# Performance work log

Hardware: AMD Instinct MI355X
Metric: run time of the kernel (lower is better)

## Reference

```python
import jax, jax.numpy as jnp
import numpy as np

N = 50000      # nodes
E = 800000     # edges
P = 100000     # pos/neg candidate edges
IN = 128       # input feat dim
H, D = 2, 64   # heads, out_feats per head
HD = H * D     # 128
NEG_SLOPE = 0.2


def setup_inputs() -> dict:
    key = jax.random.key(0)
    ks = jax.random.split(key, 18)
    def gn(k, shape, fan_in):
        return jax.random.normal(k, shape, jnp.float32) * (1.0 / np.sqrt(fan_in))
    return {
        "x": jax.random.normal(ks[0], (N, IN), jnp.float32),
        "src": jax.random.randint(ks[1], (E,), 0, N),
        "dst": jax.random.randint(ks[2], (E,), 0, N),
        "pos_src": jax.random.randint(ks[3], (P,), 0, N),
        "pos_dst": jax.random.randint(ks[4], (P,), 0, N),
        "neg_src": jax.random.randint(ks[5], (P,), 0, N),
        "neg_dst": jax.random.randint(ks[6], (P,), 0, N),
        "W0": gn(ks[7], (IN, HD), IN),
        "attn0": gn(ks[8], (H, D), D),
        "W1": gn(ks[9], (HD, HD), HD),
        "attn1": gn(ks[10], (H, D), D),
        "Wp1": gn(ks[11], (HD, D), HD),
        "bp1": jnp.zeros((D,), jnp.float32),
        "Wp2": gn(ks[12], (D, D), D),
        "bp2": jnp.zeros((D,), jnp.float32),
        "Wp3": gn(ks[13], (D, 1), D),
        "bp3": jnp.zeros((1,), jnp.float32),
    }


def gatv2_layer(h, W, attn, src, dst, residual):
    # DGL GATv2Conv, share_weights=True, bias=False, feat_drop=attn_drop=0
    feat = (h @ W).reshape(N, H, D)            # [N,H,D]
    el = feat[src]                              # [E,H,D] gather at src
    er = feat[dst]                              # [E,H,D] gather at dst
    e = jax.nn.leaky_relu(el + er, NEG_SLOPE)   # [E,H,D]
    score = jnp.einsum('ehd,hd->eh', e, attn)   # [E,H]
    # edge softmax over incoming edges of each dst node
    m = jax.ops.segment_max(score, dst, num_segments=N)      # [N,H]
    p = jnp.exp(score - m[dst])                               # [E,H]
    s = jax.ops.segment_sum(p, dst, num_segments=N)           # [N,H]
    a = p / s[dst]                                             # [E,H]
    rst = jax.ops.segment_sum(el * a[:, :, None], dst, num_segments=N)  # [N,H,D]
    if residual:
        rst = rst + h.reshape(N, H, D)          # identity res_fc (dims match)
    return jax.nn.elu(rst).reshape(N, HD)       # flatten(1)


def reference(x, src, dst, pos_src, pos_dst, neg_src, neg_dst,
              W0, attn0, W1, attn1, Wp1, bp1, Wp2, bp2, Wp3, bp3):
    h = gatv2_layer(x, W0, attn0, src, dst, residual=False)
    h = gatv2_layer(h, W1, attn1, src, dst, residual=True)

    def predictor(z):
        z = jax.nn.relu(z @ Wp1 + bp1)
        z = jax.nn.relu(z @ Wp2 + bp2)
        return z @ Wp3 + bp3

    h_pos = predictor(h[pos_src] * h[pos_dst])  # [P,1]
    h_neg = predictor(h[neg_src] * h[neg_dst])  # [P,1]
    return (h_pos, h_neg)
```

## Files before the change

### kernel.cpp

```cpp
#include <hip/hip_runtime.h>
#include <math.h>

#define NN 50000
#define NE 800000
#define NP 100000
#define NEG_SLOPE 0.2f

__device__ __forceinline__ float row_sum16(float v) {
    int x = __float_as_int(v);
    v += __int_as_float(__builtin_amdgcn_update_dpp(0, x, 0x128, 0xF, 0xF, true));
    x = __float_as_int(v);
    v += __int_as_float(__builtin_amdgcn_update_dpp(0, x, 0x124, 0xF, 0xF, true));
    x = __float_as_int(v);
    v += __int_as_float(__builtin_amdgcn_update_dpp(0, x, 0x4E, 0xF, 0xF, true));
    x = __float_as_int(v);
    v += __int_as_float(__builtin_amdgcn_update_dpp(0, x, 0xB1, 0xF, 0xF, true));
    return v;
}


__global__ void count_deg(const int* __restrict__ dst, int* __restrict__ cnt) {
    int i = blockIdx.x * blockDim.x + threadIdx.x;
    int st = gridDim.x * blockDim.x;
    for (; i < NE; i += st) atomicAdd(&cnt[dst[i]], 1);
}

__global__ __launch_bounds__(1024) void scan_deg(const int* __restrict__ cnt,
                                                 int* __restrict__ rowptr,
                                                 int* __restrict__ cursor) {
    __shared__ int wsum[16];
    __shared__ int carry;
    __shared__ int total;
    int tid = threadIdx.x;
    int lane = tid & 63, w = tid >> 6;
    if (tid == 0) carry = 0;
    __syncthreads();
    for (int base = 0; base < NN; base += 1024) {
        int idx = base + tid;
        int v = (idx < NN) ? cnt[idx] : 0;
        int x = v;
        #pragma unroll
        for (int mm = 1; mm < 64; mm <<= 1) {
            int y = __shfl_up(x, mm, 64);
            if (lane >= mm) x += y;
        }
        if (lane == 63) wsum[w] = x;
        __syncthreads();
        if (w == 0) {
            int orig = (lane < 16) ? wsum[lane] : 0;
            int t = orig;
            #pragma unroll
            for (int mm = 1; mm < 16; mm <<= 1) {
                int y = __shfl_up(t, mm, 64);
                if (lane >= mm) t += y;
            }
            if (lane < 16) wsum[lane] = t - orig;
            if (lane == 15) total = t;
        }
        __syncthreads();
        int excl = carry + wsum[w] + x - v;
        if (idx < NN) { rowptr[idx] = excl; cursor[idx] = excl; }
        __syncthreads();
        if (tid == 0) carry += total;
        __syncthreads();
    }
    if (tid == 0) rowptr[NN] = carry;
}

__global__ void scatter_edges(const int* __restrict__ src, const int* __restrict__ dst,
                              int* __restrict__ cursor, int* __restrict__ csrc) {
    int i = blockIdx.x * blockDim.x + threadIdx.x;
    int st = gridDim.x * blockDim.x;
    for (; i < NE; i += st) {
        int p = atomicAdd(&cursor[dst[i]], 1);
        csrc[p] = src[i];
    }
}


__global__ __launch_bounds__(256) void gemm128(const float* __restrict__ A,
                                               const float* __restrict__ W,
                                               float* __restrict__ out, int nrows) {
    __shared__ float Wt[128 * 132];
    __shared__ float rb[16 * 132];
    int tid = threadIdx.x;
    for (int idx = tid; idx < 128 * 128; idx += 256) {
        int k = idx >> 7, j = idx & 127;
        Wt[j * 132 + k] = W[idx];
    }
    __syncthreads();
    int lane = tid & 63, w = tid >> 6;
    int ntiles = (nrows + 15) >> 4;
    const float* w0p = &Wt[lane * 132];
    const float* w1p = &Wt[(64 + lane) * 132];
    for (int t = blockIdx.x; t < ntiles; t += gridDim.x) {
        int r0 = t << 4;
        for (int i = tid; i < 512; i += 256) {
            int rr = r0 + (i >> 5);
            float4 v = {0.f, 0.f, 0.f, 0.f};
            if (rr < nrows) v = ((const float4*)A)[(size_t)rr * 32 + (i & 31)];
            *(float4*)&rb[(i >> 5) * 132 + (i & 31) * 4] = v;
        }
        __syncthreads();
        float acc[4][2] = {};
        #pragma unroll 4
        for (int k4 = 0; k4 < 32; ++k4) {
            float4 wv0 = *(const float4*)&w0p[k4 * 4];
            float4 wv1 = *(const float4*)&w1p[k4 * 4];
            #pragma unroll
            for (int i2 = 0; i2 < 4; ++i2) {
                float4 av = *(const float4*)&rb[(w * 4 + i2) * 132 + k4 * 4];
                acc[i2][0] = fmaf(av.x, wv0.x, acc[i2][0]);
                acc[i2][0] = fmaf(av.y, wv0.y, acc[i2][0]);
                acc[i2][0] = fmaf(av.z, wv0.z, acc[i2][0]);
                acc[i2][0] = fmaf(av.w, wv0.w, acc[i2][0]);
                acc[i2][1] = fmaf(av.x, wv1.x, acc[i2][1]);
                acc[i2][1] = fmaf(av.y, wv1.y, acc[i2][1]);
                acc[i2][1] = fmaf(av.z, wv1.z, acc[i2][1]);
                acc[i2][1] = fmaf(av.w, wv1.w, acc[i2][1]);
            }
        }
        #pragma unroll
        for (int i2 = 0; i2 < 4; ++i2) {
            int rr = r0 + w * 4 + i2;
            if (rr < nrows) {
                out[(size_t)rr * 128 + lane]      = acc[i2][0];
                out[(size_t)rr * 128 + 64 + lane] = acc[i2][1];
            }
        }
        __syncthreads();
    }
}


__global__ void gat_fused(const float* __restrict__ feat,
                          const int* __restrict__ rowptr,
                          const int* __restrict__ csrc,
                          const float* __restrict__ attn,
                          const float* __restrict__ resid,
                          float* __restrict__ out) {
    int tid = blockIdx.x * blockDim.x + threadIdx.x;
    int hw = tid >> 5;
    int nhw = (gridDim.x * blockDim.x) >> 5;
    int q = threadIdx.x & 31;
    const float4* feat4 = (const float4*)feat;
    float4 at = ((const float4*)attn)[q];
    for (int d = hw; d < NN; d += nhw) {
        int beg = rowptr[d], end = rowptr[d + 1];
        float4 fd = feat4[(size_t)d * 32 + q];
        float m = 0.f, s = 0.f;
        float ax = 0.f, ay = 0.f, az = 0.f, aw = 0.f;
        bool first = true;
        int i = beg;
        float4 f0 = {0.f,0.f,0.f,0.f}, f1 = {0.f,0.f,0.f,0.f}, f2 = {0.f,0.f,0.f,0.f};
        if (i     < end) f0 = feat4[(size_t)csrc[i]     * 32 + q];
        if (i + 1 < end) f1 = feat4[(size_t)csrc[i + 1] * 32 + q];
        if (i + 2 < end) f2 = feat4[(size_t)csrc[i + 2] * 32 + q];
        int s3 = (i + 3 < end) ? csrc[i + 3] : 0;
        while (i < end) {
            float4 f3 = {0.f, 0.f, 0.f, 0.f};
            if (i + 3 < end) f3 = feat4[(size_t)s3 * 32 + q];
            int s4 = (i + 4 < end) ? csrc[i + 4] : 0;
            float ex = f0.x + fd.x; ex = ex > 0.f ? ex : NEG_SLOPE * ex;
            float ey = f0.y + fd.y; ey = ey > 0.f ? ey : NEG_SLOPE * ey;
            float ez = f0.z + fd.z; ez = ez > 0.f ? ez : NEG_SLOPE * ez;
            float ew = f0.w + fd.w; ew = ew > 0.f ? ew : NEG_SLOPE * ew;
            float part = ex * at.x + ey * at.y + ez * at.z + ew * at.w;
            part = row_sum16(part);
            float p = first ? 1.f : __expf(part - m);
            m = first ? part : m;
            first = false;
            s += p;
            ax = fmaf(f0.x, p, ax);
            ay = fmaf(f0.y, p, ay);
            az = fmaf(f0.z, p, az);
            aw = fmaf(f0.w, p, aw);
            f0 = f1; f1 = f2; f2 = f3; s3 = s4; ++i;
        }
        float inv = s > 0.f ? 1.f / s : 0.f;
        float vx = ax * inv;
        float vy = ay * inv;
        float vz = az * inv;
        float vw = aw * inv;
        if (resid) {
            float4 r = ((const float4*)resid)[(size_t)d * 32 + q];
            vx += r.x; vy += r.y; vz += r.z; vw += r.w;
        }
        vx = vx > 0.f ? vx : expm1f(vx);
        vy = vy > 0.f ? vy : expm1f(vy);
        vz = vz > 0.f ? vz : expm1f(vz);
        vw = vw > 0.f ? vw : expm1f(vw);
        float4 o; o.x = vx; o.y = vy; o.z = vz; o.w = vw;
        ((float4*)out)[(size_t)d * 32 + q] = o;
    }
}


__global__ __launch_bounds__(512, 1) void predictor(const float* __restrict__ h,
                          const int* __restrict__ ps, const int* __restrict__ pd,
                          const int* __restrict__ ns, const int* __restrict__ nd,
                          const float* __restrict__ Wp1, const float* __restrict__ bp1,
                          const float* __restrict__ Wp2, const float* __restrict__ bp2,
                          const float* __restrict__ Wp3, const float* __restrict__ bp3,
                          float* __restrict__ out) {
    __shared__ float S[29696];
    int tid = threadIdx.x;
    for (int idx = tid; idx < 128 * 64; idx += 512) {
        int k = idx >> 6, c = idx & 63;
        S[c * 132 + k] = Wp1[idx];
    }
    for (int idx = tid; idx < 64 * 64; idx += 512) {
        int k = idx >> 6, c = idx & 63;
        S[8448 + c * 68 + k] = Wp2[idx];
    }
    __syncthreads();
    int lane = tid & 63;
    int w = tid >> 6;
    int cg = lane & 15, rg = lane >> 4;
    float* zz = S + 12800 + w * 2112;
    float b1v[4], b2v[4], w3v[4];
    #pragma unroll
    for (int i = 0; i < 4; ++i) {
        b1v[i] = bp1[cg + 16 * i];
        b2v[i] = bp2[cg + 16 * i];
        w3v[i] = Wp3[cg + 16 * i];
    }
    float b3 = bp3[0];
    int gw = blockIdx.x * 8 + w;
    int gnw = gridDim.x * 8;
    int ge = lane >> 2, gp = lane & 3;
    const float4* h4 = (const float4*)h;
    const int NT = (2 * NP) / 16;
    for (int T = gw; T < NT; T += gnw) {
        int e = T * 16 + ge;
        int a, b;
        if (e < NP) { a = ps[e]; b = pd[e]; }
        else        { a = ns[e - NP]; b = nd[e - NP]; }
        const float4* pa = h4 + (size_t)a * 32 + gp;
        const float4* pb = h4 + (size_t)b * 32 + gp;
        #pragma unroll
        for (int qq = 0; qq < 8; ++qq) {
            float4 va = pa[qq * 4];
            float4 vb = pb[qq * 4];
            float4 vz;
            vz.x = va.x * vb.x; vz.y = va.y * vb.y;
            vz.z = va.z * vb.z; vz.w = va.w * vb.w;
            *(float4*)&zz[ge * 132 + gp * 4 + qq * 16] = vz;
        }
        float acc[4][4] = {};
        #pragma unroll 4
        for (int k4 = 0; k4 < 32; ++k4) {
            float4 wv[4], zv[4];
            #pragma unroll
            for (int i = 0; i < 4; ++i)
                wv[i] = *(const float4*)&S[(cg + 16 * i) * 132 + k4 * 4];
            #pragma unroll
            for (int j = 0; j < 4; ++j)
                zv[j] = *(const float4*)&zz[(rg * 4 + j) * 132 + k4 * 4];
            #pragma unroll
            for (int j = 0; j < 4; ++j) {
                #pragma unroll
                for (int i = 0; i < 4; ++i) {
                    acc[j][i] = fmaf(zv[j].x, wv[i].x, acc[j][i]);
                    acc[j][i] = fmaf(zv[j].y, wv[i].y, acc[j][i]);
                    acc[j][i] = fmaf(zv[j].z, wv[i].z, acc[j][i]);
                    acc[j][i] = fmaf(zv[j].w, wv[i].w, acc[j][i]);
                }
            }
        }
        #pragma unroll
        for (int j = 0; j < 4; ++j) {
            #pragma unroll
            for (int i = 0; i < 4; ++i)
                zz[(rg * 4 + j) * 68 + cg + 16 * i] = fmaxf(acc[j][i] + b1v[i], 0.f);
        }
        float acc2[4][4] = {};
        #pragma unroll 4
        for (int k4 = 0; k4 < 16; ++k4) {
            float4 wv[4], zv[4];
            #pragma unroll
            for (int i = 0; i < 4; ++i)
                wv[i] = *(const float4*)&S[8448 + (cg + 16 * i) * 68 + k4 * 4];
            #pragma unroll
            for (int j = 0; j < 4; ++j)
                zv[j] = *(const float4*)&zz[(rg * 4 + j) * 68 + k4 * 4];
            #pragma unroll
            for (int j = 0; j < 4; ++j) {
                #pragma unroll
                for (int i = 0; i < 4; ++i) {
                    acc2[j][i] = fmaf(zv[j].x, wv[i].x, acc2[j][i]);
                    acc2[j][i] = fmaf(zv[j].y, wv[i].y, acc2[j][i]);
                    acc2[j][i] = fmaf(zv[j].z, wv[i].z, acc2[j][i]);
                    acc2[j][i] = fmaf(zv[j].w, wv[i].w, acc2[j][i]);
                }
            }
        }
        float v[4];
        #pragma unroll
        for (int j = 0; j < 4; ++j) {
            float sv = 0.f;
            #pragma unroll
            for (int i = 0; i < 4; ++i)
                sv = fmaf(fmaxf(acc2[j][i] + b2v[i], 0.f), w3v[i], sv);
            v[j] = row_sum16(sv);
        }
        if (cg == 0) {
            float4 o;
            o.x = v[0] + b3; o.y = v[1] + b3; o.z = v[2] + b3; o.w = v[3] + b3;
            *(float4*)&out[T * 16 + rg * 4] = o;
        }
    }
}

extern "C" void kernel_launch(void* const* d_in, const int* in_sizes, int n_in,
                              void* d_out, int out_size, void* d_ws, size_t ws_size,
                              hipStream_t stream) {
    const float* x       = (const float*)d_in[0];
    const int*   src     = (const int*)d_in[1];
    const int*   dst     = (const int*)d_in[2];
    const int*   pos_src = (const int*)d_in[3];
    const int*   pos_dst = (const int*)d_in[4];
    const int*   neg_src = (const int*)d_in[5];
    const int*   neg_dst = (const int*)d_in[6];
    const float* W0      = (const float*)d_in[7];
    const float* attn0   = (const float*)d_in[8];
    const float* W1      = (const float*)d_in[9];
    const float* attn1   = (const float*)d_in[10];
    const float* Wp1     = (const float*)d_in[11];
    const float* bp1     = (const float*)d_in[12];
    const float* Wp2     = (const float*)d_in[13];
    const float* bp2     = (const float*)d_in[14];
    const float* Wp3     = (const float*)d_in[15];
    const float* bp3     = (const float*)d_in[16];

    float* A = (float*)d_ws;
    float* B = A + (size_t)NN * 128;
    float* C = B + (size_t)NN * 128;
    int* cnt    = (int*)(C + (size_t)NN * 128);
    int* rowptr = cnt + NN;
    int* cursor = rowptr + NN + 1;
    int* csrc   = cursor + NN;
    float* out = (float*)d_out;

    hipMemsetAsync(cnt, 0, NN * sizeof(int), stream);
    count_deg<<<3125, 256, 0, stream>>>(dst, cnt);
    scan_deg<<<1, 1024, 0, stream>>>(cnt, rowptr, cursor);
    scatter_edges<<<3125, 256, 0, stream>>>(src, dst, cursor, csrc);

    gemm128<<<1024, 256, 0, stream>>>(x, W0, A, NN);
    gat_fused<<<3125, 256, 0, stream>>>(A, rowptr, csrc, attn0, nullptr, C);

    gemm128<<<1024, 256, 0, stream>>>(C, W1, A, NN);
    gat_fused<<<3125, 256, 0, stream>>>(A, rowptr, csrc, attn1, C, B);

    predictor<<<256, 512, 0, stream>>>(B, pos_src, pos_dst, neg_src, neg_dst,
                                       Wp1, bp1, Wp2, bp2, Wp3, bp3, out);
}
```

Measured before the change: 440.3 us.

## Parallelize degree scan, vectorize CSR build, unroll GAT edge loop by four

Replaces the single-block serial degree scan with a three-kernel multi-block scan (partial sums, top-level scan, apply). The degree count and edge scatter now read src/dst as int4, with a quarter as many threads. The GAT aggregation loop peels the first edge to drop the per-edge 'first' branch, uses fmaxf for leaky ReLU, and unrolls the main loop by four with deeper index prefetch. The aim is to remove the serial scan latency and some loop overhead, at the cost of two extra kernel launches and extra workspace for the partial sums.

```diff
diff --git a/kernel.cpp b/kernel.cpp
--- a/kernel.cpp
+++ b/kernel.cpp
@@ -5,6 +5,7 @@
 #define NE 800000
 #define NP 100000
 #define NEG_SLOPE 0.2f
+#define SCAN_NB 196
 
 __device__ __forceinline__ float row_sum16(float v) {
     int x = __float_as_int(v);
@@ -22,58 +23,86 @@
 __global__ void count_deg(const int* __restrict__ dst, int* __restrict__ cnt) {
     int i = blockIdx.x * blockDim.x + threadIdx.x;
     int st = gridDim.x * blockDim.x;
-    for (; i < NE; i += st) atomicAdd(&cnt[dst[i]], 1);
-}
-
-__global__ __launch_bounds__(1024) void scan_deg(const int* __restrict__ cnt,
-                                                 int* __restrict__ rowptr,
-                                                 int* __restrict__ cursor) {
-    __shared__ int wsum[16];
-    __shared__ int carry;
-    __shared__ int total;
-    int tid = threadIdx.x;
-    int lane = tid & 63, w = tid >> 6;
-    if (tid == 0) carry = 0;
+    const int4* d4 = (const int4*)dst;
+    for (; i < NE / 4; i += st) {
+        int4 d = d4[i];
+        atomicAdd(&cnt[d.x], 1);
+        atomicAdd(&cnt[d.y], 1);
+        atomicAdd(&cnt[d.z], 1);
+        atomicAdd(&cnt[d.w], 1);
+    }
+}
+
+__global__ __launch_bounds__(256) void scan_part(const int* __restrict__ cnt,
+                                                 int* __restrict__ partial) {
+    __shared__ int ws[4];
+    int t = threadIdx.x;
+    int idx = blockIdx.x * 256 + t;
+    int v = (idx < NN) ? cnt[idx] : 0;
+    #pragma unroll
+    for (int mm = 1; mm < 64; mm <<= 1) v += __shfl_xor(v, mm, 64);
+    if ((t & 63) == 0) ws[t >> 6] = v;
     __syncthreads();
-    for (int base = 0; base < NN; base += 1024) {
-        int idx = base + tid;
-        int v = (idx < NN) ? cnt[idx] : 0;
-        int x = v;
-        #pragma unroll
-        for (int mm = 1; mm < 64; mm <<= 1) {
-            int y = __shfl_up(x, mm, 64);
-            if (lane >= mm) x += y;
-        }
-        if (lane == 63) wsum[w] = x;
-        __syncthreads();
-        if (w == 0) {
-            int orig = (lane < 16) ? wsum[lane] : 0;
-            int t = orig;
-            #pragma unroll
-            for (int mm = 1; mm < 16; mm <<= 1) {
-                int y = __shfl_up(t, mm, 64);
-                if (lane >= mm) t += y;
-            }
-            if (lane < 16) wsum[lane] = t - orig;
-            if (lane == 15) total = t;
-        }
-        __syncthreads();
-        int excl = carry + wsum[w] + x - v;
-        if (idx < NN) { rowptr[idx] = excl; cursor[idx] = excl; }
-        __syncthreads();
-        if (tid == 0) carry += total;
-        __syncthreads();
-    }
-    if (tid == 0) rowptr[NN] = carry;
+    if (t == 0) partial[blockIdx.x] = ws[0] + ws[1] + ws[2] + ws[3];
+}
+
+__global__ __launch_bounds__(256) void scan_top(const int* __restrict__ partial,
+                                                int* __restrict__ partoff,
+                                                int* __restrict__ rowptr) {
+    __shared__ int wsum[4];
+    int t = threadIdx.x, lane = t & 63, w = t >> 6;
+    int v = (t < SCAN_NB) ? partial[t] : 0;
+    int x = v;
+    #pragma unroll
+    for (int mm = 1; mm < 64; mm <<= 1) {
+        int y = __shfl_up(x, mm, 64);
+        if (lane >= mm) x += y;
+    }
+    if (lane == 63) wsum[w] = x;
+    __syncthreads();
+    int off = 0;
+    for (int k = 0; k < w; ++k) off += wsum[k];
+    int excl = off + x - v;
+    if (t < SCAN_NB) partoff[t] = excl;
+    if (t == SCAN_NB - 1) rowptr[NN] = excl + v;
+}
+
+__global__ __launch_bounds__(256) void scan_apply(const int* __restrict__ cnt,
+                                                  const int* __restrict__ partoff,
+                                                  int* __restrict__ rowptr,
+                                                  int* __restrict__ cursor) {
+    __shared__ int wsum[4];
+    int t = threadIdx.x, lane = t & 63, w = t >> 6;
+    int idx = blockIdx.x * 256 + t;
+    int v = (idx < NN) ? cnt[idx] : 0;
+    int x = v;
+    #pragma unroll
+    for (int mm = 1; mm < 64; mm <<= 1) {
+        int y = __shfl_up(x, mm, 64);
+        if (lane >= mm) x += y;
+    }
+    if (lane == 63) wsum[w] = x;
+    __syncthreads();
+    int off = partoff[blockIdx.x];
+    for (int k = 0; k < w; ++k) off += wsum[k];
+    int excl = off + x - v;
+    if (idx < NN) { rowptr[idx] = excl; cursor[idx] = excl; }
 }
 
 __global__ void scatter_edges(const int* __restrict__ src, const int* __restrict__ dst,
                               int* __restrict__ cursor, int* __restrict__ csrc) {
     int i = blockIdx.x * blockDim.x + threadIdx.x;
     int st = gridDim.x * blockDim.x;
-    for (; i < NE; i += st) {
-        int p = atomicAdd(&cursor[dst[i]], 1);
-        csrc[p] = src[i];
+    const int4* s4 = (const int4*)src;
+    const int4* d4 = (const int4*)dst;
+    for (; i < NE / 4; i += st) {
+        int4 s = s4[i];
+        int4 d = d4[i];
+        int p;
+        p = atomicAdd(&cursor[d.x], 1); csrc[p] = s.x;
+        p = atomicAdd(&cursor[d.y], 1); csrc[p] = s.y;
+        p = atomicAdd(&cursor[d.z], 1); csrc[p] = s.z;
+        p = atomicAdd(&cursor[d.w], 1); csrc[p] = s.w;
     }
 }
 
@@ -132,6 +161,21 @@
     }
 }
 
+
+#define GAT_EDGE(fv) do {                                          \
+    float ex = fv.x + fd.x; ex = fmaxf(ex, NEG_SLOPE * ex);        \
+    float ey = fv.y + fd.y; ey = fmaxf(ey, NEG_SLOPE * ey);        \
+    float ez = fv.z + fd.z; ez = fmaxf(ez, NEG_SLOPE * ez);        \
+    float ew = fv.w + fd.w; ew = fmaxf(ew, NEG_SLOPE * ew);        \
+    float part = ex * at.x + ey * at.y + ez * at.z + ew * at.w;    \
+    part = row_sum16(part);                                        \
+    float p = __expf(part - m);                                    \
+    s += p;                                                        \
+    ax = fmaf(fv.x, p, ax);                                        \
+    ay = fmaf(fv.y, p, ay);                                        \
+    az = fmaf(fv.z, p, az);                                        \
+    aw = fmaf(fv.w, p, aw);                                        \
+} while (0)
 
 __global__ void gat_fused(const float* __restrict__ feat,
                           const int* __restrict__ rowptr,
@@ -150,31 +194,50 @@
         float4 fd = feat4[(size_t)d * 32 + q];
         float m = 0.f, s = 0.f;
         float ax = 0.f, ay = 0.f, az = 0.f, aw = 0.f;
-        bool first = true;
         int i = beg;
         float4 f0 = {0.f,0.f,0.f,0.f}, f1 = {0.f,0.f,0.f,0.f}, f2 = {0.f,0.f,0.f,0.f};
-        if (i     < end) f0 = feat4[(size_t)csrc[i]     * 32 + q];
-        if (i + 1 < end) f1 = feat4[(size_t)csrc[i + 1] * 32 + q];
-        if (i + 2 < end) f2 = feat4[(size_t)csrc[i + 2] * 32 + q];
-        int s3 = (i + 3 < end) ? csrc[i + 3] : 0;
+        int s3 = 0;
+        if (i < end) {
+            int p0 = csrc[i];
+            int p1 = (i + 1 < end) ? csrc[i + 1] : 0;
+            int p2 = (i + 2 < end) ? csrc[i + 2] : 0;
+            int p3 = (i + 3 < end) ? csrc[i + 3] : 0;
+            s3     = (i + 4 < end) ? csrc[i + 4] : 0;
+            float4 fp = feat4[(size_t)p0 * 32 + q];
+            if (i + 1 < end) f0 = feat4[(size_t)p1 * 32 + q];
+            if (i + 2 < end) f1 = feat4[(size_t)p2 * 32 + q];
+            if (i + 3 < end) f2 = feat4[(size_t)p3 * 32 + q];
+            float ex = fp.x + fd.x; ex = fmaxf(ex, NEG_SLOPE * ex);
+            float ey = fp.y + fd.y; ey = fmaxf(ey, NEG_SLOPE * ey);
+            float ez = fp.z + fd.z; ez = fmaxf(ez, NEG_SLOPE * ez);
+            float ew = fp.w + fd.w; ew = fmaxf(ew, NEG_SLOPE * ew);
+            float part = ex * at.x + ey * at.y + ez * at.z + ew * at.w;
+            m = row_sum16(part);
+            s = 1.f;
+            ax = fp.x; ay = fp.y; az = fp.z; aw = fp.w;
+            ++i;
+        }
+        while (i + 8 <= end) {
+            int s4 = csrc[i + 4];
+            int s5 = csrc[i + 5];
+            int s6 = csrc[i + 6];
+            int s7 = csrc[i + 7];
+            float4 f3 = feat4[(size_t)s3 * 32 + q];
+            GAT_EDGE(f0);
+            f0 = feat4[(size_t)s4 * 32 + q];
+            GAT_EDGE(f1);
+            f1 = feat4[(size_t)s5 * 32 + q];
+            GAT_EDGE(f2);
+            f2 = feat4[(size_t)s6 * 32 + q];
+            GAT_EDGE(f3);
+            s3 = s7;
+            i += 4;
+        }
         while (i < end) {
             float4 f3 = {0.f, 0.f, 0.f, 0.f};
             if (i + 3 < end) f3 = feat4[(size_t)s3 * 32 + q];
             int s4 = (i + 4 < end) ? csrc[i + 4] : 0;
-            float ex = f0.x + fd.x; ex = ex > 0.f ? ex : NEG_SLOPE * ex;
-            float ey = f0.y + fd.y; ey = ey > 0.f ? ey : NEG_SLOPE * ey;
-            float ez = f0.z + fd.z; ez = ez > 0.f ? ez : NEG_SLOPE * ez;
-            float ew = f0.w + fd.w; ew = ew > 0.f ? ew : NEG_SLOPE * ew;
-            float part = ex * at.x + ey * at.y + ez * at.z + ew * at.w;
-            part = row_sum16(part);
-            float p = first ? 1.f : __expf(part - m);
-            m = first ? part : m;
-            first = false;
-            s += p;
-            ax = fmaf(f0.x, p, ax);
-            ay = fmaf(f0.y, p, ay);
-            az = fmaf(f0.z, p, az);
-            aw = fmaf(f0.w, p, aw);
+            GAT_EDGE(f0);
             f0 = f1; f1 = f2; f2 = f3; s3 = s4; ++i;
         }
         float inv = s > 0.f ? 1.f / s : 0.f;
@@ -336,16 +399,20 @@
     float* A = (float*)d_ws;
     float* B = A + (size_t)NN * 128;
     float* C = B + (size_t)NN * 128;
-    int* cnt    = (int*)(C + (size_t)NN * 128);
-    int* rowptr = cnt + NN;
-    int* cursor = rowptr + NN + 1;
-    int* csrc   = cursor + NN;
+    int* cnt     = (int*)(C + (size_t)NN * 128);
+    int* rowptr  = cnt + NN;
+    int* cursor  = rowptr + NN + 1;
+    int* csrc    = cursor + NN;
+    int* partial = csrc + NE;
+    int* partoff = partial + SCAN_NB;
     float* out = (float*)d_out;
 
     hipMemsetAsync(cnt, 0, NN * sizeof(int), stream);
-    count_deg<<<3125, 256, 0, stream>>>(dst, cnt);
-    scan_deg<<<1, 1024, 0, stream>>>(cnt, rowptr, cursor);
-    scatter_edges<<<3125, 256, 0, stream>>>(src, dst, cursor, csrc);
+    count_deg<<<782, 256, 0, stream>>>(dst, cnt);
+    scan_part<<<SCAN_NB, 256, 0, stream>>>(cnt, partial);
+    scan_top<<<1, 256, 0, stream>>>(partial, partoff, rowptr);
+    scan_apply<<<SCAN_NB, 256, 0, stream>>>(cnt, partoff, rowptr, cursor);
+    scatter_edges<<<782, 256, 0, stream>>>(src, dst, cursor, csrc);
 
     gemm128<<<1024, 256, 0, stream>>>(x, W0, A, NN);
     gat_fused<<<3125, 256, 0, stream>>>(A, rowptr, csrc, attn0, nullptr, C);
```

Result: faster. 388.9 us (-11.7%).
